# Performance work log

Hardware: AMD Instinct MI355X
Metric: run time of the kernel (lower is better)

The kernel has to match this reference:

```python
import jax, jax.numpy as jnp
import numpy as np

NUM_EMBEDDINGS = 8192
EMBEDDING_DIM = 256
PROJECTION_DIM = 128


def setup_inputs() -> dict:
    key = jax.random.key(0)
    k_x, k_cb, k_w, k_b = jax.random.split(key, 4)
    x = jax.random.normal(k_x, (16, 1024, EMBEDDING_DIM), dtype=jnp.float32)
    codebook = jax.random.normal(k_cb, (NUM_EMBEDDINGS, EMBEDDING_DIM), dtype=jnp.float32)
    proj_w = jax.random.normal(k_w, (EMBEDDING_DIM, PROJECTION_DIM), dtype=jnp.float32) / np.sqrt(EMBEDDING_DIM)
    proj_b = jax.random.normal(k_b, (PROJECTION_DIM,), dtype=jnp.float32) * 0.01
    return {"x": x, "codebook": codebook, "proj_w": proj_w, "proj_b": proj_b}


def reference(x, codebook, proj_w, proj_b):
    # Flatten tokens: [N, D]
    x_flat = x.reshape(-1, EMBEDDING_DIM)
    # Project tokens and codebook into the distance space: [N, P], [K, P]
    x_proj = x_flat @ proj_w + proj_b
    cb_proj = codebook @ proj_w + proj_b
    # Squared euclidean distances via expansion: [N, K]
    distances = (
        jnp.sum(x_proj ** 2, axis=1, keepdims=True)
        - 2.0 * (x_proj @ cb_proj.T)
        + jnp.sum(cb_proj ** 2, axis=1)
    )
    idx = jnp.argmin(distances, axis=1)
    discrete = jax.nn.one_hot(idx, NUM_EMBEDDINGS, dtype=x.dtype)  # [N, K]
    # One-hot matmul lookup (disguised gather): [N, D]
    quantized = (discrete @ codebook).reshape(x.shape)
    return (discrete, quantized)
```

## Files before the change

kernel.cpp:

```cpp
#include <hip/hip_runtime.h>
#include <math.h>

#define D 256
#define P 128
#define K 8192
#define NTOK 16384
#define NROWS (NTOK + K)
#define NCHUNK 8
#define KCHUNK (K / NCHUNK)
#define CAP 15
#define MARGIN 3.0f
#define FLT_BIG 3.402823466e+38f

typedef __attribute__((ext_vector_type(8))) short bf16x8;
typedef __attribute__((ext_vector_type(4))) float f32x4;
typedef __attribute__((ext_vector_type(8))) unsigned short u16x8;

__device__ __forceinline__ unsigned short f32_to_bf16_rne(float f) {
    unsigned int u = __float_as_uint(f);
    u = (u + 0x7fffu + ((u >> 16) & 1u)) >> 16;
    return (unsigned short)u;
}

__global__ __launch_bounds__(256) void zero_kernel(float4* __restrict__ p, size_t n4) {
    size_t i = (size_t)blockIdx.x * blockDim.x + threadIdx.x;
    size_t stride = (size_t)gridDim.x * blockDim.x;
    float4 z; z.x = 0.f; z.y = 0.f; z.z = 0.f; z.w = 0.f;
    for (; i < n4; i += stride) p[i] = z;
}

__global__ __launch_bounds__(256) void proj_kernel(
    const float* __restrict__ x, const float* __restrict__ cb,
    const float* __restrict__ w, const float* __restrict__ bias,
    float* __restrict__ xproj, float* __restrict__ cproj,
    float* __restrict__ xnorm, float* __restrict__ cnorm,
    unsigned short* __restrict__ xh, unsigned short* __restrict__ ch)
{
    __shared__ float As[16][D];
    const int tid = threadIdx.x;
    const int row0 = blockIdx.x * 16;

    for (int i = tid; i < 16 * (D / 4); i += 256) {
        int r = i / (D / 4);
        int c4 = i % (D / 4);
        int gr = row0 + r;
        const float* src = (gr < NTOK) ? (x + (size_t)gr * D)
                                       : (cb + (size_t)(gr - NTOK) * D);
        float4 v = ((const float4*)src)[c4];
        ((float4*)&As[r][0])[c4] = v;
    }
    __syncthreads();

    const int r = tid >> 4;
    const int c0 = (tid & 15) * 8;

    float acc[8];
#pragma unroll
    for (int j = 0; j < 8; j++) acc[j] = 0.f;

    for (int d = 0; d < D; d += 4) {
        float4 a4 = *(const float4*)&As[r][d];
#pragma unroll
        for (int dd = 0; dd < 4; dd++) {
            float av = (dd == 0) ? a4.x : (dd == 1) ? a4.y : (dd == 2) ? a4.z : a4.w;
            float4 w0 = *(const float4*)&w[(size_t)(d + dd) * P + c0];
            float4 w1 = *(const float4*)&w[(size_t)(d + dd) * P + c0 + 4];
            acc[0] = fmaf(av, w0.x, acc[0]);
            acc[1] = fmaf(av, w0.y, acc[1]);
            acc[2] = fmaf(av, w0.z, acc[2]);
            acc[3] = fmaf(av, w0.w, acc[3]);
            acc[4] = fmaf(av, w1.x, acc[4]);
            acc[5] = fmaf(av, w1.y, acc[5]);
            acc[6] = fmaf(av, w1.z, acc[6]);
            acc[7] = fmaf(av, w1.w, acc[7]);
        }
    }

    float out[8];
    float nrm = 0.f;
    u16x8 hv;
#pragma unroll
    for (int j = 0; j < 8; j++) {
        out[j] = acc[j] + bias[c0 + j];
        nrm = fmaf(out[j], out[j], nrm);
        hv[j] = f32_to_bf16_rne(out[j]);
    }

    const int gr = row0 + r;
    float* dst;
    unsigned short* hdst;
    if (gr < NTOK) { dst = xproj + (size_t)gr * P; hdst = xh + (size_t)gr * P; }
    else           { dst = cproj + (size_t)(gr - NTOK) * P; hdst = ch + (size_t)(gr - NTOK) * P; }
    float4 o0; o0.x = out[0]; o0.y = out[1]; o0.z = out[2]; o0.w = out[3];
    float4 o1; o1.x = out[4]; o1.y = out[5]; o1.z = out[6]; o1.w = out[7];
    *(float4*)&dst[c0] = o0;
    *(float4*)&dst[c0 + 4] = o1;
    *(u16x8*)&hdst[c0] = hv;

#pragma unroll
    for (int off = 1; off < 16; off <<= 1)
        nrm += __shfl_xor(nrm, off, 16);
    if ((tid & 15) == 0) {
        if (gr < NTOK) xnorm[gr] = nrm;
        else           cnorm[gr - NTOK] = nrm;
    }
}

__global__ __launch_bounds__(256) void filter_kernel(
    const unsigned short* __restrict__ xh, const unsigned short* __restrict__ ch,
    const float* __restrict__ xnorm, const float* __restrict__ cnorm,
    float* __restrict__ chunkmin, int* __restrict__ cand)
{
    __shared__ short sb[64][136];
    __shared__ float smin[128];
    __shared__ int scnt[128];
    __shared__ int scand[128][CAP];

    const int tid = threadIdx.x;
    const int tok0 = blockIdx.x * 128;
    const int chunk = blockIdx.y;
    const int k0 = chunk * KCHUNK;

    const int wave = tid >> 6;
    const int lane = tid & 63;
    const int quad = lane >> 4;
    const int l15 = lane & 15;

    if (tid < 128) scnt[tid] = 0;

    bf16x8 afrag[2][4];
#pragma unroll
    for (int mi = 0; mi < 2; mi++)
#pragma unroll
        for (int ks = 0; ks < 4; ks++)
            afrag[mi][ks] = *(const bf16x8*)(
                xh + (size_t)(tok0 + wave * 32 + mi * 16 + l15) * P + ks * 32 + quad * 8);

    float xnv[2][4];
#pragma unroll
    for (int mi = 0; mi < 2; mi++)
#pragma unroll
        for (int r = 0; r < 4; r++)
            xnv[mi][r] = xnorm[tok0 + wave * 32 + mi * 16 + quad * 4 + r];

    float rmin[2][4];
#pragma unroll
    for (int mi = 0; mi < 2; mi++)
#pragma unroll
        for (int r = 0; r < 4; r++) rmin[mi][r] = FLT_BIG;

    for (int ct = 0; ct < KCHUNK / 64; ct++) {
        const int kt = k0 + ct * 64;
        __syncthreads();
        for (int i = tid; i < 64 * 16; i += 256) {
            int row = i >> 4;
            int c8 = i & 15;
            uint4 v = *(const uint4*)(ch + (size_t)(kt + row) * P + c8 * 8);
            *(uint4*)&sb[row][c8 * 8] = v;
        }
        __syncthreads();

        f32x4 acc[2][4];
#pragma unroll
        for (int mi = 0; mi < 2; mi++)
#pragma unroll
            for (int nj = 0; nj < 4; nj++)
                acc[mi][nj] = (f32x4)(0.f);

#pragma unroll
        for (int ks = 0; ks < 4; ks++) {
            const int kf = ks * 32 + quad * 8;
            bf16x8 b0 = *(const bf16x8*)&sb[l15][kf];
            bf16x8 b1 = *(const bf16x8*)&sb[16 + l15][kf];
            bf16x8 b2 = *(const bf16x8*)&sb[32 + l15][kf];
            bf16x8 b3 = *(const bf16x8*)&sb[48 + l15][kf];
            acc[0][0] = __builtin_amdgcn_mfma_f32_16x16x32_bf16(afrag[0][ks], b0, acc[0][0], 0, 0, 0);
            acc[0][1] = __builtin_amdgcn_mfma_f32_16x16x32_bf16(afrag[0][ks], b1, acc[0][1], 0, 0, 0);
            acc[0][2] = __builtin_amdgcn_mfma_f32_16x16x32_bf16(afrag[0][ks], b2, acc[0][2], 0, 0, 0);
            acc[0][3] = __builtin_amdgcn_mfma_f32_16x16x32_bf16(afrag[0][ks], b3, acc[0][3], 0, 0, 0);
            acc[1][0] = __builtin_amdgcn_mfma_f32_16x16x32_bf16(afrag[1][ks], b0, acc[1][0], 0, 0, 0);
            acc[1][1] = __builtin_amdgcn_mfma_f32_16x16x32_bf16(afrag[1][ks], b1, acc[1][1], 0, 0, 0);
            acc[1][2] = __builtin_amdgcn_mfma_f32_16x16x32_bf16(afrag[1][ks], b2, acc[1][2], 0, 0, 0);
            acc[1][3] = __builtin_amdgcn_mfma_f32_16x16x32_bf16(afrag[1][ks], b3, acc[1][3], 0, 0, 0);
        }

        float cn[4];
#pragma unroll
        for (int nj = 0; nj < 4; nj++) cn[nj] = cnorm[kt + nj * 16 + l15];

#pragma unroll
        for (int mi = 0; mi < 2; mi++)
#pragma unroll
            for (int r = 0; r < 4; r++) {
                float d[4];
#pragma unroll
                for (int nj = 0; nj < 4; nj++)
                    d[nj] = (xnv[mi][r] - 2.0f * acc[mi][nj][r]) + cn[nj];
                float m = fminf(fminf(d[0], d[1]), fminf(d[2], d[3]));
#pragma unroll
                for (int off = 1; off < 16; off <<= 1)
                    m = fminf(m, __shfl_xor(m, off));
                float rm = fminf(rmin[mi][r], m);
                rmin[mi][r] = rm;
                float thr = rm + MARGIN;
                int tl = wave * 32 + mi * 16 + quad * 4 + r;
#pragma unroll
                for (int nj = 0; nj < 4; nj++) {
                    if (d[nj] <= thr) {
                        int pos = atomicAdd(&scnt[tl], 1);
                        if (pos < CAP)
                            scand[tl][pos] = kt + nj * 16 + l15;
                    }
                }
            }
    }

    if (l15 == 0) {
#pragma unroll
        for (int mi = 0; mi < 2; mi++)
#pragma unroll
            for (int r = 0; r < 4; r++)
                smin[wave * 32 + mi * 16 + quad * 4 + r] = rmin[mi][r];
    }
    __syncthreads();

    if (tid < 128) {
        int t = tok0 + tid;
        int cnt = scnt[tid];
        if (cnt > CAP) cnt = CAP;
        int* rec = cand + ((size_t)t * NCHUNK + chunk) * (CAP + 1);
        rec[0] = cnt;
        for (int j = 0; j < cnt; j++) rec[1 + j] = scand[tid][j];
        chunkmin[(size_t)t * NCHUNK + chunk] = smin[tid];
    }
}

__global__ __launch_bounds__(256) void rescore_kernel(
    const float* __restrict__ xproj, const float* __restrict__ cproj,
    const float* __restrict__ xnorm, const float* __restrict__ cnorm,
    const float* __restrict__ chunkmin, const int* __restrict__ cand,
    int* __restrict__ fidx)
{
    const int tid = threadIdx.x;
    const int lane = tid & 63;
    const int wave = tid >> 6;
    const int t = blockIdx.x * 4 + wave;

    float cm = (lane < NCHUNK) ? chunkmin[(size_t)t * NCHUNK + lane] : FLT_BIG;
#pragma unroll
    for (int off = 1; off < 8; off <<= 1)
        cm = fminf(cm, __shfl_xor(cm, off));
    float mg = __shfl(cm, 0);

    const float xn = xnorm[t];
    float bv = FLT_BIG;
    int bi = 0x7fffffff;

    for (int c = 0; c < NCHUNK; c++) {
        if (chunkmin[(size_t)t * NCHUNK + c] > mg + MARGIN) continue;
        const int* rec = cand + ((size_t)t * NCHUNK + c) * (CAP + 1);
        int cnt = rec[0];
        for (int j = 0; j < cnt; j++) {
            if (((c * CAP + j) & 63) != lane) continue;
            int k = rec[1 + j];
            const float* xr = xproj + (size_t)t * P;
            const float* cr = cproj + (size_t)k * P;
            float s = 0.f;
            for (int p = 0; p < P; p += 4) {
                float4 a = *(const float4*)&xr[p];
                float4 b = *(const float4*)&cr[p];
                s = fmaf(a.x, b.x, s);
                s = fmaf(a.y, b.y, s);
                s = fmaf(a.z, b.z, s);
                s = fmaf(a.w, b.w, s);
            }
            float dist = (xn - 2.0f * s) + cnorm[k];
            if (dist < bv || (dist == bv && k < bi)) { bv = dist; bi = k; }
        }
    }

#pragma unroll
    for (int off = 1; off < 64; off <<= 1) {
        float ov = __shfl_xor(bv, off);
        int oi = __shfl_xor(bi, off);
        if (ov < bv || (ov == bv && oi < bi)) { bv = ov; bi = oi; }
    }
    if (lane == 0) fidx[t] = bi;
}

__global__ __launch_bounds__(256) void finalize_kernel(
    const int* __restrict__ fidx, const float* __restrict__ cb,
    float* __restrict__ discrete, float* __restrict__ quant)
{
    __shared__ int sidx[64];
    const int tid = threadIdx.x;
    const int tok0 = blockIdx.x * 64;

    if (tid < 64) {
        int t = tok0 + tid;
        int bi = fidx[t];
        sidx[tid] = bi;
        discrete[(size_t)t * K + bi] = 1.0f;
    }
    __syncthreads();

    for (int i = tid; i < 64 * (D / 4); i += 256) {
        int t = i >> 6;
        int c4 = i & 63;
        int bi = sidx[t];
        float4 v = ((const float4*)(cb + (size_t)bi * D))[c4];
        ((float4*)(quant + (size_t)(tok0 + t) * D))[c4] = v;
    }
}

extern "C" void kernel_launch(void* const* d_in, const int* in_sizes, int n_in,
                              void* d_out, int out_size, void* d_ws, size_t ws_size,
                              hipStream_t stream) {
    const float* x    = (const float*)d_in[0];
    const float* cb   = (const float*)d_in[1];
    const float* w    = (const float*)d_in[2];
    const float* bias = (const float*)d_in[3];

    float* out = (float*)d_out;
    float* discrete = out;
    float* quant = out + (size_t)NTOK * K;

    char* ws = (char*)d_ws;
    size_t off = 0;
    float* xproj = (float*)(ws + off); off += (size_t)NTOK * P * 4;
    float* cproj = (float*)(ws + off); off += (size_t)K * P * 4;
    float* xnorm = (float*)(ws + off); off += (size_t)NTOK * 4;
    float* cnorm = (float*)(ws + off); off += (size_t)K * 4;
    unsigned short* xh = (unsigned short*)(ws + off); off += (size_t)NTOK * P * 2;
    unsigned short* ch = (unsigned short*)(ws + off); off += (size_t)K * P * 2;
    float* chunkmin = (float*)(ws + off); off += (size_t)NTOK * NCHUNK * 4;
    int* cand = (int*)(ws + off); off += (size_t)NTOK * NCHUNK * (CAP + 1) * 4;
    int* fidx = (int*)(ws + off); off += (size_t)NTOK * 4;

    zero_kernel<<<dim3(8192), dim3(256), 0, stream>>>(
        (float4*)discrete, (size_t)NTOK * K / 4);

    proj_kernel<<<dim3(NROWS / 16), dim3(256), 0, stream>>>(
        x, cb, w, bias, xproj, cproj, xnorm, cnorm, xh, ch);

    filter_kernel<<<dim3(NTOK / 128, NCHUNK), dim3(256), 0, stream>>>(
        xh, ch, xnorm, cnorm, chunkmin, cand);

    rescore_kernel<<<dim3(NTOK / 4), dim3(256), 0, stream>>>(
        xproj, cproj, xnorm, cnorm, chunkmin, cand, fidx);

    finalize_kernel<<<dim3(NTOK / 64), dim3(256), 0, stream>>>(
        fidx, cb, discrete, quant);
}
```

Measured before the change: 1.010 ms.

## Fuse candidate rescoring into filter kernel via packed 64-bit atomicMin

Removes the separate rescore kernel and the per-chunk candidate buffers. Each filter lane that finds a candidate within the margin now computes the exact fp32 distance inline and does an atomicMin on a per-token 64-bit key packing distance bits and index. The per-token key is initialised in the projection kernel. This drops one launch, the candidate write/read traffic and the capacity limit. The cost is divergent scalar dot products inside the bf16 MFMA loop, and the packed ordering relies on distances being non-negative.

```diff
diff --git a/kernel.cpp b/kernel.cpp
--- a/kernel.cpp
+++ b/kernel.cpp
@@ -8,7 +8,6 @@
 #define NROWS (NTOK + K)
 #define NCHUNK 8
 #define KCHUNK (K / NCHUNK)
-#define CAP 15
 #define MARGIN 3.0f
 #define FLT_BIG 3.402823466e+38f
 
@@ -34,11 +33,17 @@
     const float* __restrict__ w, const float* __restrict__ bias,
     float* __restrict__ xproj, float* __restrict__ cproj,
     float* __restrict__ xnorm, float* __restrict__ cnorm,
-    unsigned short* __restrict__ xh, unsigned short* __restrict__ ch)
+    unsigned short* __restrict__ xh, unsigned short* __restrict__ ch,
+    unsigned long long* __restrict__ best)
 {
     __shared__ float As[16][D];
     const int tid = threadIdx.x;
     const int row0 = blockIdx.x * 16;
+
+    {
+        int g = blockIdx.x * 256 + tid;
+        if (g < NTOK) best[g] = 0xFFFFFFFFFFFFFFFFull;
+    }
 
     for (int i = tid; i < 16 * (D / 4); i += 256) {
         int r = i / (D / 4);
@@ -109,24 +114,19 @@
 __global__ __launch_bounds__(256) void filter_kernel(
     const unsigned short* __restrict__ xh, const unsigned short* __restrict__ ch,
     const float* __restrict__ xnorm, const float* __restrict__ cnorm,
-    float* __restrict__ chunkmin, int* __restrict__ cand)
+    const float* __restrict__ xproj, const float* __restrict__ cproj,
+    unsigned long long* __restrict__ best)
 {
     __shared__ short sb[64][136];
-    __shared__ float smin[128];
-    __shared__ int scnt[128];
-    __shared__ int scand[128][CAP];
 
     const int tid = threadIdx.x;
     const int tok0 = blockIdx.x * 128;
-    const int chunk = blockIdx.y;
-    const int k0 = chunk * KCHUNK;
+    const int k0 = blockIdx.y * KCHUNK;
 
     const int wave = tid >> 6;
     const int lane = tid & 63;
     const int quad = lane >> 4;
     const int l15 = lane & 15;
-
-    if (tid < 128) scnt[tid] = 0;
 
     bf16x8 afrag[2][4];
 #pragma unroll
@@ -203,93 +203,36 @@
                 float rm = fminf(rmin[mi][r], m);
                 rmin[mi][r] = rm;
                 float thr = rm + MARGIN;
-                int tl = wave * 32 + mi * 16 + quad * 4 + r;
+                const int tok = tok0 + wave * 32 + mi * 16 + quad * 4 + r;
 #pragma unroll
                 for (int nj = 0; nj < 4; nj++) {
                     if (d[nj] <= thr) {
-                        int pos = atomicAdd(&scnt[tl], 1);
-                        if (pos < CAP)
-                            scand[tl][pos] = kt + nj * 16 + l15;
+                        int k = kt + nj * 16 + l15;
+                        const float* xr = xproj + (size_t)tok * P;
+                        const float* cr = cproj + (size_t)k * P;
+                        float s = 0.f;
+#pragma unroll 4
+                        for (int p = 0; p < P; p += 4) {
+                            float4 a = *(const float4*)&xr[p];
+                            float4 b = *(const float4*)&cr[p];
+                            s = fmaf(a.x, b.x, s);
+                            s = fmaf(a.y, b.y, s);
+                            s = fmaf(a.z, b.z, s);
+                            s = fmaf(a.w, b.w, s);
+                        }
+                        float dist = (xnv[mi][r] - 2.0f * s) + cn[nj];
+                        unsigned long long pack =
+                            ((unsigned long long)__float_as_uint(dist) << 32) |
+                            (unsigned long long)(unsigned)k;
+                        atomicMin(&best[tok], pack);
                     }
                 }
             }
     }
-
-    if (l15 == 0) {
-#pragma unroll
-        for (int mi = 0; mi < 2; mi++)
-#pragma unroll
-            for (int r = 0; r < 4; r++)
-                smin[wave * 32 + mi * 16 + quad * 4 + r] = rmin[mi][r];
-    }
-    __syncthreads();
-
-    if (tid < 128) {
-        int t = tok0 + tid;
-        int cnt = scnt[tid];
-        if (cnt > CAP) cnt = CAP;
-        int* rec = cand + ((size_t)t * NCHUNK + chunk) * (CAP + 1);
-        rec[0] = cnt;
-        for (int j = 0; j < cnt; j++) rec[1 + j] = scand[tid][j];
-        chunkmin[(size_t)t * NCHUNK + chunk] = smin[tid];
-    }
-}
-
-__global__ __launch_bounds__(256) void rescore_kernel(
-    const float* __restrict__ xproj, const float* __restrict__ cproj,
-    const float* __restrict__ xnorm, const float* __restrict__ cnorm,
-    const float* __restrict__ chunkmin, const int* __restrict__ cand,
-    int* __restrict__ fidx)
-{
-    const int tid = threadIdx.x;
-    const int lane = tid & 63;
-    const int wave = tid >> 6;
-    const int t = blockIdx.x * 4 + wave;
-
-    float cm = (lane < NCHUNK) ? chunkmin[(size_t)t * NCHUNK + lane] : FLT_BIG;
-#pragma unroll
-    for (int off = 1; off < 8; off <<= 1)
-        cm = fminf(cm, __shfl_xor(cm, off));
-    float mg = __shfl(cm, 0);
-
-    const float xn = xnorm[t];
-    float bv = FLT_BIG;
-    int bi = 0x7fffffff;
-
-    for (int c = 0; c < NCHUNK; c++) {
-        if (chunkmin[(size_t)t * NCHUNK + c] > mg + MARGIN) continue;
-        const int* rec = cand + ((size_t)t * NCHUNK + c) * (CAP + 1);
-        int cnt = rec[0];
-        for (int j = 0; j < cnt; j++) {
-            if (((c * CAP + j) & 63) != lane) continue;
-            int k = rec[1 + j];
-            const float* xr = xproj + (size_t)t * P;
-            const float* cr = cproj + (size_t)k * P;
-            float s = 0.f;
-            for (int p = 0; p < P; p += 4) {
-                float4 a = *(const float4*)&xr[p];
-                float4 b = *(const float4*)&cr[p];
-                s = fmaf(a.x, b.x, s);
-                s = fmaf(a.y, b.y, s);
-                s = fmaf(a.z, b.z, s);
-                s = fmaf(a.w, b.w, s);
-            }
-            float dist = (xn - 2.0f * s) + cnorm[k];
-            if (dist < bv || (dist == bv && k < bi)) { bv = dist; bi = k; }
-        }
-    }
-
-#pragma unroll
-    for (int off = 1; off < 64; off <<= 1) {
-        float ov = __shfl_xor(bv, off);
-        int oi = __shfl_xor(bi, off);
-        if (ov < bv || (ov == bv && oi < bi)) { bv = ov; bi = oi; }
-    }
-    if (lane == 0) fidx[t] = bi;
 }
 
 __global__ __launch_bounds__(256) void finalize_kernel(
-    const int* __restrict__ fidx, const float* __restrict__ cb,
+    const unsigned long long* __restrict__ best, const float* __restrict__ cb,
     float* __restrict__ discrete, float* __restrict__ quant)
 {
     __shared__ int sidx[64];
@@ -298,7 +241,7 @@
 
     if (tid < 64) {
         int t = tok0 + tid;
-        int bi = fidx[t];
+        int bi = (int)(best[t] & 0xFFFFFFFFull);
         sidx[tid] = bi;
         discrete[(size_t)t * K + bi] = 1.0f;
     }
@@ -333,22 +276,17 @@
     float* cnorm = (float*)(ws + off); off += (size_t)K * 4;
     unsigned short* xh = (unsigned short*)(ws + off); off += (size_t)NTOK * P * 2;
     unsigned short* ch = (unsigned short*)(ws + off); off += (size_t)K * P * 2;
-    float* chunkmin = (float*)(ws + off); off += (size_t)NTOK * NCHUNK * 4;
-    int* cand = (int*)(ws + off); off += (size_t)NTOK * NCHUNK * (CAP + 1) * 4;
-    int* fidx = (int*)(ws + off); off += (size_t)NTOK * 4;
+    unsigned long long* best = (unsigned long long*)(ws + off); off += (size_t)NTOK * 8;
 
     zero_kernel<<<dim3(8192), dim3(256), 0, stream>>>(
         (float4*)discrete, (size_t)NTOK * K / 4);
 
     proj_kernel<<<dim3(NROWS / 16), dim3(256), 0, stream>>>(
-        x, cb, w, bias, xproj, cproj, xnorm, cnorm, xh, ch);
+        x, cb, w, bias, xproj, cproj, xnorm, cnorm, xh, ch, best);
 
     filter_kernel<<<dim3(NTOK / 128, NCHUNK), dim3(256), 0, stream>>>(
-        xh, ch, xnorm, cnorm, chunkmin, cand);
-
-    rescore_kernel<<<dim3(NTOK / 4), dim3(256), 0, stream>>>(
-        xproj, cproj, xnorm, cnorm, chunkmin, cand, fidx);
+        xh, ch, xnorm, cnorm, xproj, cproj, best);
 
     finalize_kernel<<<dim3(NTOK / 64), dim3(256), 0, stream>>>(
-        fidx, cb, discrete, quant);
-}
+        best, cb, discrete, quant);
+}
```

Result: slower. 1.653 ms (+63.7%).
